# Kernel tuning notes

Measured on AMD Instinct MI355X. Metric: run time of the kernel, lower is better.

The kernel has to match this reference:

```python
import jax, jax.numpy as jnp
import numpy as np

B, D, HGT, WID = 32, 512, 8, 32   # batch, channels, feature map H, W
T = HGT * WID                     # 256 spatial tokens
NH, L, MAXLEN = 8, 2, 25          # heads, encoder layers, max text len


def _ln(x, s, b, eps=1e-5):
    m = jnp.mean(x, -1, keepdims=True)
    v = jnp.mean((x - m) ** 2, -1, keepdims=True)
    return (x - m) * jax.lax.rsqrt(v + eps) * s + b


def setup_inputs() -> dict:
    key = jax.random.key(0)
    ks = jax.random.split(key, 16)
    w = lambda k, shp: jax.random.normal(k, shp, jnp.float32) * 0.02
    return {
        "x": jax.random.normal(ks[0], (B, D, HGT, WID), jnp.float32),
        "encoder_word_pos": jnp.arange(T, dtype=jnp.int32),
        "gsrm_word_pos": jnp.arange(MAXLEN, dtype=jnp.int32),
        # encoder positional table
        "pos_table": w(ks[1], (T, D)),
        # per-layer encoder params (stacked over L)
        "ln1_s": jnp.ones((L, D), jnp.float32), "ln1_b": jnp.zeros((L, D), jnp.float32),
        "Wq": w(ks[2], (L, D, D)), "bq": jnp.zeros((L, D), jnp.float32),
        "Wk": w(ks[3], (L, D, D)), "bk": jnp.zeros((L, D), jnp.float32),
        "Wv": w(ks[4], (L, D, D)), "bv": jnp.zeros((L, D), jnp.float32),
        "Wo": w(ks[5], (L, D, D)), "bo": jnp.zeros((L, D), jnp.float32),
        "ln2_s": jnp.ones((L, D), jnp.float32), "ln2_b": jnp.zeros((L, D), jnp.float32),
        "W1": w(ks[6], (L, D, D)), "b1": jnp.zeros((L, D), jnp.float32),  # d_inner_hid = hidden_dim
        "W2": w(ks[7], (L, D, D)), "b2": jnp.zeros((L, D), jnp.float32),
        "lnf_s": jnp.ones((D,), jnp.float32), "lnf_b": jnp.zeros((D,), jnp.float32),
        # PVAM head params
        "fc0_w": w(ks[8], (D, D)), "fc0_b": jnp.zeros((D,), jnp.float32),
        "emb_table": w(ks[9], (MAXLEN, D)),
        "fc1_w": w(ks[10], (D,)),
    }


def _pvam(x, encoder_word_pos, gsrm_word_pos, pos_table,
          ln1_s, ln1_b, Wq, bq, Wk, bk, Wv, bv, Wo, bo,
          ln2_s, ln2_b, W1, b1, W2, b2, lnf_s, lnf_b,
          fc0_w, fc0_b, emb_table, fc1_w):
    b, c, h, wd = x.shape
    feat = x.reshape(b, c, h * wd).transpose(0, 2, 1)          # [b, t, c]
    # prepare encoder: scale + learned positional embedding (eval mode: no dropout)
    enc = feat * jnp.sqrt(jnp.float32(c)) + pos_table[encoder_word_pos]
    dk = c // NH
    scale = 1.0 / jnp.sqrt(jnp.float32(dk))
    for l in range(L):  # pre-norm transformer encoder (preprocess='n', postprocess='da')
        qin = _ln(enc, ln1_s[l], ln1_b[l])
        q = (qin @ Wq[l] + bq[l]).reshape(b, -1, NH, dk)
        k = (qin @ Wk[l] + bk[l]).reshape(b, -1, NH, dk)
        v = (qin @ Wv[l] + bv[l]).reshape(b, -1, NH, dk)
        p = jax.nn.softmax(jnp.einsum('bqhd,bkhd->bhqk', q, k) * scale, -1)
        o = jnp.einsum('bhqk,bkhd->bqhd', p, v).reshape(b, -1, c)
        enc = enc + (o @ Wo[l] + bo[l])
        y = _ln(enc, ln2_s[l], ln2_b[l])
        enc = enc + (jax.nn.relu(y @ W1[l] + b1[l]) @ W2[l] + b2[l])
    enc = _ln(enc, lnf_s, lnf_b)
    word_features = enc @ fc0_w + fc0_b                        # [b, t, c]
    word_pos = emb_table[gsrm_word_pos]                        # [max_len, c]
    # additive attention: tanh(broadcast add) -> scalar score -> softmax over t
    y = jnp.tanh(word_features[:, None, :, :] + word_pos[None, :, None, :])  # [b,max_len,t,c]
    attn = jax.nn.softmax(jnp.einsum('bmtc,c->bmt', y, fc1_w), -1)
    return jnp.einsum('bmt,btc->bmc', attn, word_features)    # [b, max_len, c]


def reference(x, encoder_word_pos, gsrm_word_pos, pos_table,
              ln1_s, ln1_b, Wq, bq, Wk, bk, Wv, bv, Wo, bo,
              ln2_s, ln2_b, W1, b1, W2, b2, lnf_s, lnf_b,
              fc0_w, fc0_b, emb_table, fc1_w):
    return _pvam(x, encoder_word_pos, gsrm_word_pos, pos_table,
                 ln1_s, ln1_b, Wq, bq, Wk, bk, Wv, bv, Wo, bo,
                 ln2_s, ln2_b, W1, b1, W2, b2, lnf_s, lnf_b,
                 fc0_w, fc0_b, emb_table, fc1_w)
```

## Files before the change

### kernel.cpp

```cpp
#include <hip/hip_runtime.h>
#include <math.h>

#define B_ 32
#define D_ 512
#define T_ 256
#define NH_ 8
#define DK_ 64
#define ML_ 25

typedef unsigned short ushort_t;
using short8 = __attribute__((ext_vector_type(8))) short;
using f32x4  = __attribute__((ext_vector_type(4))) float;

__device__ __forceinline__ ushort_t f2bf(float f) {
    unsigned u = __float_as_uint(f);
    unsigned r = (u + 0x7fffu + ((u >> 16) & 1u)) >> 16;
    return (ushort_t)r;
}
__device__ __forceinline__ float bf2f(ushort_t h) {
    return __uint_as_float(((unsigned)h) << 16);
}
__device__ __forceinline__ void gl16(const void* g, void* l) {
    __builtin_amdgcn_global_load_lds((const __attribute__((address_space(1))) void*)g,
                                     (__attribute__((address_space(3))) void*)l, 16, 0, 0);
}
#define ZERO4(v) { (v)[0]=0.f; (v)[1]=0.f; (v)[2]=0.f; (v)[3]=0.f; }

__global__ __launch_bounds__(256) void prep_kernel(const float* __restrict__ x,
                                                   const int* __restrict__ epos,
                                                   const float* __restrict__ pos,
                                                   float* __restrict__ enc) {
    __shared__ float ld[64][65];
    int tt = blockIdx.x, ct = blockIdx.y, b = blockIdx.z;
    int t0 = tt * 64, c0 = ct * 64;
    int tid = threadIdx.x;
    int r = tid >> 4, c4 = (tid & 15) << 2;
#pragma unroll
    for (int p = 0; p < 4; p++) {
        int row = p * 16 + r;
        float4 v = *(const float4*)(x + ((size_t)(b * D_ + c0 + row) * T_ + t0) + c4);
        ld[row][c4 + 0] = v.x; ld[row][c4 + 1] = v.y; ld[row][c4 + 2] = v.z; ld[row][c4 + 3] = v.w;
    }
    __syncthreads();
#pragma unroll
    for (int p = 0; p < 4; p++) {
        int tr = p * 16 + r;
        int ep = epos[t0 + tr];
        float4 pv = *(const float4*)(pos + (size_t)ep * D_ + c0 + c4);
        float4 o;
        o.x = ld[c4 + 0][tr] * 22.627417f + pv.x;
        o.y = ld[c4 + 1][tr] * 22.627417f + pv.y;
        o.z = ld[c4 + 2][tr] * 22.627417f + pv.z;
        o.w = ld[c4 + 3][tr] * 22.627417f + pv.w;
        *(float4*)(enc + (size_t)(b * T_ + t0 + tr) * D_ + c0 + c4) = o;
    }
}

__global__ __launch_bounds__(256) void convert_w_kernel(const float* __restrict__ Wq,
                                                        const float* __restrict__ Wk,
                                                        const float* __restrict__ Wv,
                                                        const float* __restrict__ Wo,
                                                        const float* __restrict__ W1,
                                                        const float* __restrict__ W2,
                                                        const float* __restrict__ fc0,
                                                        ushort_t* __restrict__ wt) {
    __shared__ float ld[64][65];
    int m = blockIdx.x >> 6;
    int tile = blockIdx.x & 63;
    int tn = tile >> 3, tk = tile & 7;
    int n0 = tn * 64, k0 = tk * 64;
    const float* src;
    if (m < 12) {
        int l = m / 6, w = m % 6;
        const float* bases[6] = {Wq, Wk, Wv, Wo, W1, W2};
        src = bases[w] + (size_t)l * D_ * D_;
    } else {
        src = fc0;
    }
    int tid = threadIdx.x;
    int r = tid >> 4, c4 = (tid & 15) << 2;
#pragma unroll
    for (int p = 0; p < 4; p++) {
        int row = p * 16 + r;
        float4 v = *(const float4*)(src + (size_t)(k0 + row) * D_ + n0 + c4);
        ld[row][c4 + 0] = v.x; ld[row][c4 + 1] = v.y; ld[row][c4 + 2] = v.z; ld[row][c4 + 3] = v.w;
    }
    __syncthreads();
    ushort_t* dsth = wt + (size_t)m * D_ * D_;
    ushort_t* dstl = wt + (size_t)13 * D_ * D_;
#pragma unroll
    for (int p = 0; p < 4; p++) {
        int n = p * 16 + r;
        int kc = c4;
        ushort_t h[4], lo[4];
#pragma unroll
        for (int i = 0; i < 4; i++) {
            float f = ld[kc + i][n];
            h[i] = f2bf(f);
            lo[i] = f2bf(f - bf2f(h[i]));
        }
        *(ushort4*)(dsth + (size_t)(n0 + n) * D_ + k0 + kc) = make_ushort4(h[0], h[1], h[2], h[3]);
        if (m == 12)
            *(ushort4*)(dstl + (size_t)(n0 + n) * D_ + k0 + kc) = make_ushort4(lo[0], lo[1], lo[2], lo[3]);
    }
}

template<bool LO>
__global__ __launch_bounds__(256) void ln_kernel(const float* __restrict__ x,
                                                 const float* __restrict__ s,
                                                 const float* __restrict__ b,
                                                 ushort_t* __restrict__ yh,
                                                 ushort_t* __restrict__ yl) {
    int wid = threadIdx.x >> 6, lane = threadIdx.x & 63;
    size_t row = (size_t)blockIdx.x * 4 + wid;
    const float4* xr = (const float4*)(x + row * D_);
    float4 v0 = xr[lane * 2], v1 = xr[lane * 2 + 1];
    float sum = v0.x + v0.y + v0.z + v0.w + v1.x + v1.y + v1.z + v1.w;
    for (int o = 32; o; o >>= 1) sum += __shfl_xor(sum, o);
    float mean = sum * (1.f / 512.f);
    float d[8] = {v0.x - mean, v0.y - mean, v0.z - mean, v0.w - mean,
                  v1.x - mean, v1.y - mean, v1.z - mean, v1.w - mean};
    float vs = 0.f;
#pragma unroll
    for (int i = 0; i < 8; i++) vs += d[i] * d[i];
    for (int o = 32; o; o >>= 1) vs += __shfl_xor(vs, o);
    float rs = 1.f / sqrtf(vs * (1.f / 512.f) + 1e-5f);
    const float4* s4 = (const float4*)s;
    const float4* b4 = (const float4*)b;
    float4 sa = s4[lane * 2], sb = s4[lane * 2 + 1];
    float4 ba = b4[lane * 2], bb = b4[lane * 2 + 1];
    float o8[8];
    o8[0] = d[0] * rs * sa.x + ba.x; o8[1] = d[1] * rs * sa.y + ba.y;
    o8[2] = d[2] * rs * sa.z + ba.z; o8[3] = d[3] * rs * sa.w + ba.w;
    o8[4] = d[4] * rs * sb.x + bb.x; o8[5] = d[5] * rs * sb.y + bb.y;
    o8[6] = d[6] * rs * sb.z + bb.z; o8[7] = d[7] * rs * sb.w + bb.w;
    ushort_t h[8];
#pragma unroll
    for (int i = 0; i < 8; i++) h[i] = f2bf(o8[i]);
    uint4 u;
    u.x = (unsigned)h[0] | ((unsigned)h[1] << 16);
    u.y = (unsigned)h[2] | ((unsigned)h[3] << 16);
    u.z = (unsigned)h[4] | ((unsigned)h[5] << 16);
    u.w = (unsigned)h[6] | ((unsigned)h[7] << 16);
    *(uint4*)(yh + row * D_ + lane * 8) = u;
    if (LO) {
        ushort_t l8[8];
#pragma unroll
        for (int i = 0; i < 8; i++) l8[i] = f2bf(o8[i] - bf2f(h[i]));
        uint4 ul;
        ul.x = (unsigned)l8[0] | ((unsigned)l8[1] << 16);
        ul.y = (unsigned)l8[2] | ((unsigned)l8[3] << 16);
        ul.z = (unsigned)l8[4] | ((unsigned)l8[5] << 16);
        ul.w = (unsigned)l8[6] | ((unsigned)l8[7] << 16);
        *(uint4*)(yl + row * D_ + lane * 8) = ul;
    }
}

template<int EPI>
__global__ __launch_bounds__(256) void gemm_kernel(const ushort_t* __restrict__ A0,
                                                   const ushort_t* __restrict__ A1,
                                                   const ushort_t* __restrict__ A2,
                                                   const ushort_t* __restrict__ B0,
                                                   const ushort_t* __restrict__ B1,
                                                   const ushort_t* __restrict__ B2,
                                                   int nseg, int nbn,
                                                   const float* __restrict__ bias,
                                                   const float* __restrict__ bias2,
                                                   const float* __restrict__ bias3,
                                                   const float* __restrict__ res,
                                                   float* __restrict__ outF,
                                                   ushort_t* __restrict__ outB) {
    __shared__ ushort_t As[3][128 * 64];
    __shared__ ushort_t Bs[3][64 * 64];
    int tid = threadIdx.x;
    int g = blockIdx.x;
    int per = gridDim.x >> 3;
    int lin = (g & 7) * per + (g >> 3);
    int bm = lin / nbn, bn = lin % nbn;

    int lane = tid & 63;
    int wid = tid >> 6;
    int wm = wid >> 1, wn = wid & 1;
    int xr = (lane & 7) << 3;

    f32x4 acc[4][2];
#pragma unroll
    for (int i = 0; i < 4; i++)
#pragma unroll
        for (int j = 0; j < 2; j++) ZERO4(acc[i][j]);

    int nt = nseg * 8;

#define STAGE(kt, buf)                                                                  \
    {                                                                                   \
        int seg_ = (kt) >> 3;                                                           \
        int k0_ = ((kt) & 7) * 64;                                                      \
        const ushort_t* Asg = seg_ == 0 ? A0 : (seg_ == 1 ? A1 : A2);                   \
        const ushort_t* Bsg = seg_ == 0 ? B0 : (seg_ == 1 ? B1 : B2);                   \
        _Pragma("unroll")                                                               \
        for (int it = 0; it < 4; it++) {                                                \
            int uu = tid + it * 256;                                                    \
            int row_ = uu >> 3;                                                         \
            int kb_ = (((uu & 7) ^ (row_ & 7)) << 3);                                   \
            gl16(Asg + (size_t)(bm * 128 + row_) * 512 + k0_ + kb_, &As[buf][uu * 8]);  \
        }                                                                               \
        _Pragma("unroll")                                                               \
        for (int it = 0; it < 2; it++) {                                                \
            int uu = tid + it * 256;                                                    \
            int row_ = uu >> 3;                                                         \
            int kb_ = (((uu & 7) ^ (row_ & 7)) << 3);                                   \
            gl16(Bsg + (size_t)(bn * 64 + row_) * 512 + k0_ + kb_, &Bs[buf][uu * 8]);   \
        }                                                                               \
    }

#define COMPUTE(bufc)                                                                        \
    {                                                                                        \
        _Pragma("unroll")                                                                    \
        for (int kc = 0; kc < 2; kc++) {                                                     \
            short8 a[4], b[2];                                                               \
            int koff = (kc * 32 + ((lane >> 4) << 3)) ^ xr;                                  \
            _Pragma("unroll")                                                                \
            for (int i = 0; i < 4; i++)                                                      \
                a[i] = *(const short8*)&As[bufc][(wm * 64 + i * 16 + (lane & 15)) * 64 + koff]; \
            _Pragma("unroll")                                                                \
            for (int j = 0; j < 2; j++)                                                      \
                b[j] = *(const short8*)&Bs[bufc][(wn * 32 + j * 16 + (lane & 15)) * 64 + koff]; \
            _Pragma("unroll")                                                                \
            for (int i = 0; i < 4; i++)                                                      \
                _Pragma("unroll")                                                            \
                for (int j = 0; j < 2; j++)                                                  \
                    acc[i][j] = __builtin_amdgcn_mfma_f32_16x16x32_bf16(a[i], b[j], acc[i][j], 0, 0, 0); \
        }                                                                                    \
    }

    STAGE(0, 0);
    if (nt > 1) STAGE(1, 1);
    asm volatile("s_waitcnt vmcnt(6)" ::: "memory");
    __builtin_amdgcn_s_barrier();

    int cur = 0;
    for (int t = 0; t < nt; t++) {
        if (t + 2 < nt) STAGE(t + 2, (cur + 2 >= 3 ? cur - 1 : cur + 2));
        COMPUTE(cur);
        if (t + 2 < nt) {
            asm volatile("s_waitcnt vmcnt(6)" ::: "memory");
        } else if (t + 1 < nt) {
            asm volatile("s_waitcnt vmcnt(0)" ::: "memory");
        }
        __builtin_amdgcn_s_barrier();
        cur = (cur == 2) ? 0 : cur + 1;
    }
#undef STAGE
#undef COMPUTE

#pragma unroll
    for (int i = 0; i < 4; i++) {
#pragma unroll
        for (int j = 0; j < 2; j++) {
            int r0 = bm * 128 + wm * 64 + i * 16 + ((lane >> 4) << 2);
            int col = bn * 64 + wn * 32 + j * 16 + (lane & 15);
            int seg = col >> 9;
            int ccol = col & 511;
            const float* bp = bias;
            if (EPI == 5) bp = (seg == 0) ? bias : (seg == 1 ? bias2 : bias3);
            float bc = bp[EPI == 5 ? ccol : col];
#pragma unroll
            for (int jj = 0; jj < 4; jj++) {
                float v = acc[i][j][jj] + bc;
                int row = r0 + jj;
                size_t idx = (size_t)row * 512 + col;
                if (EPI == 2) {
                    outF[idx] = v + res[idx];
                } else if (EPI == 3) {
                    outB[idx] = f2bf(fmaxf(v, 0.f));
                } else if (EPI == 4) {
                    outF[idx] = v;
                } else if (EPI == 5) {
                    if (seg < 2) {
                        outB[(size_t)seg * 4194304 + (size_t)row * 512 + ccol] = f2bf(v);
                    } else {
                        int bb2 = row >> 8, t2 = row & 255;
                        outB[(size_t)2 * 4194304 +
                             ((size_t)(bb2 * 8 + (ccol >> 6)) * 64 + (ccol & 63)) * 256 + t2] = f2bf(v);
                    }
                }
            }
        }
    }
}

__global__ __launch_bounds__(256) void attn_fused_kernel(const ushort_t* __restrict__ q,
                                                         const ushort_t* __restrict__ k,
                                                         const ushort_t* __restrict__ vt,
                                                         ushort_t* __restrict__ ao) {
    __shared__ ushort_t KVs[256 * 64];
    __shared__ ushort_t Ps[64 * 256];
    int tid = threadIdx.x;
    int lane = tid & 63;
    int wid = tid >> 6;
    int m0 = blockIdx.x * 64;
    int bh = blockIdx.y;
    int b = bh >> 3, h = bh & 7;
    int xr = (lane & 7) << 3;

#pragma unroll
    for (int it = 0; it < 8; it++) {
        int uu = tid + it * 256;
        int row = uu >> 3;
        int gx = ((uu & 7) ^ (row & 7)) << 3;
        gl16(k + (size_t)(b * T_ + row) * D_ + h * DK_ + gx, &KVs[uu * 8]);
    }
    short8 qa0, qa1;
    {
        int qrow = m0 + wid * 16 + (lane & 15);
        const ushort_t* qp = q + (size_t)(b * T_ + qrow) * D_ + h * DK_ + ((lane >> 4) << 3);
        qa0 = *(const short8*)(qp);
        qa1 = *(const short8*)(qp + 32);
    }
    f32x4 acc[16];
#pragma unroll
    for (int j = 0; j < 16; j++) ZERO4(acc[j]);
    asm volatile("s_waitcnt vmcnt(0)" ::: "memory");
    __syncthreads();

#pragma unroll
    for (int j = 0; j < 16; j++) {
        int krow = j * 16 + (lane & 15);
        short8 b0 = *(const short8*)&KVs[krow * 64 + ((((lane >> 4) << 3)) ^ xr)];
        short8 b1 = *(const short8*)&KVs[krow * 64 + ((32 + ((lane >> 4) << 3)) ^ xr)];
        acc[j] = __builtin_amdgcn_mfma_f32_16x16x32_bf16(qa0, b0, acc[j], 0, 0, 0);
        acc[j] = __builtin_amdgcn_mfma_f32_16x16x32_bf16(qa1, b1, acc[j], 0, 0, 0);
    }
    __syncthreads();

#pragma unroll
    for (int it = 0; it < 8; it++) {
        int uu = tid + it * 256;
        int row = uu >> 5;
        int gx = ((uu & 31) ^ (row & 7)) << 3;
        gl16(vt + ((size_t)bh * DK_ + row) * T_ + gx, &KVs[uu * 8]);
    }

    const float C = 0.125f * 1.44269504f;
#pragma unroll
    for (int jj = 0; jj < 4; jj++) {
        float mx = -1e30f;
#pragma unroll
        for (int j = 0; j < 16; j++) mx = fmaxf(mx, acc[j][jj]);
#pragma unroll
        for (int msk = 1; msk < 16; msk <<= 1) mx = fmaxf(mx, __shfl_xor(mx, msk));
        float sm = 0.f;
#pragma unroll
        for (int j = 0; j < 16; j++) {
            float e = __builtin_amdgcn_exp2f((acc[j][jj] - mx) * C);
            acc[j][jj] = e;
            sm += e;
        }
#pragma unroll
        for (int msk = 1; msk < 16; msk <<= 1) sm += __shfl_xor(sm, msk);
        float inv = 1.f / sm;
#pragma unroll
        for (int j = 0; j < 16; j++) acc[j][jj] *= inv;
    }
#pragma unroll
    for (int j = 0; j < 16; j++) {
#pragma unroll
        for (int jj = 0; jj < 4; jj++) {
            int row = wid * 16 + ((lane >> 4) << 2) + jj;
            int col = j * 16 + (lane & 15);
            Ps[row * 256 + (col ^ ((row & 7) << 3))] = f2bf(acc[j][jj]);
        }
    }
    asm volatile("s_waitcnt vmcnt(0)" ::: "memory");
    __syncthreads();

    int wm = wid >> 1, wn = wid & 1;
    f32x4 acc2[2][2];
#pragma unroll
    for (int i = 0; i < 2; i++)
#pragma unroll
        for (int j = 0; j < 2; j++) ZERO4(acc2[i][j]);
#pragma unroll
    for (int kc = 0; kc < 8; kc++) {
        int off = (kc * 32 + ((lane >> 4) << 3)) ^ xr;
        short8 a0 = *(const short8*)&Ps[(wm * 32 + (lane & 15)) * 256 + off];
        short8 a1 = *(const short8*)&Ps[(wm * 32 + 16 + (lane & 15)) * 256 + off];
        short8 b0 = *(const short8*)&KVs[(wn * 32 + (lane & 15)) * 256 + off];
        short8 b1 = *(const short8*)&KVs[(wn * 32 + 16 + (lane & 15)) * 256 + off];
        acc2[0][0] = __builtin_amdgcn_mfma_f32_16x16x32_bf16(a0, b0, acc2[0][0], 0, 0, 0);
        acc2[0][1] = __builtin_amdgcn_mfma_f32_16x16x32_bf16(a0, b1, acc2[0][1], 0, 0, 0);
        acc2[1][0] = __builtin_amdgcn_mfma_f32_16x16x32_bf16(a1, b0, acc2[1][0], 0, 0, 0);
        acc2[1][1] = __builtin_amdgcn_mfma_f32_16x16x32_bf16(a1, b1, acc2[1][1], 0, 0, 0);
    }
#pragma unroll
    for (int i = 0; i < 2; i++)
#pragma unroll
        for (int j = 0; j < 2; j++)
#pragma unroll
            for (int jj = 0; jj < 4; jj++)
                ao[(size_t)(b * T_ + m0 + wm * 32 + i * 16 + ((lane >> 4) << 2) + jj) * D_ +
                   h * DK_ + wn * 32 + j * 16 + (lane & 15)] = f2bf(acc2[i][j][jj]);
}

__global__ __launch_bounds__(256) void scores_kernel(const float* __restrict__ wf,
                                                     const int* __restrict__ gpos,
                                                     const float* __restrict__ emb,
                                                     const float* __restrict__ w1,
                                                     float* __restrict__ scores) {
    __shared__ float wpL[5][512];
    __shared__ float w1m2[512];
    const float K2 = 2.885390082f;
    int tid = threadIdx.x;
    int b = blockIdx.y;
    int mg = blockIdx.z * 5;
    int t = blockIdx.x * 32 + (tid >> 3);
    int cg = tid & 7;
    for (int idx = tid; idx < 5 * 128; idx += 256) {
        int m = idx >> 7, w4 = idx & 127;
        float4 v = *(const float4*)(emb + (size_t)gpos[mg + m] * D_ + (w4 << 2));
        v.x *= K2; v.y *= K2; v.z *= K2; v.w *= K2;
        *(float4*)&wpL[m][w4 << 2] = v;
    }
    if (tid < 128) {
        float4 v = *(const float4*)(w1 + (tid << 2));
        v.x *= -2.f; v.y *= -2.f; v.z *= -2.f; v.w *= -2.f;
        *(float4*)&w1m2[tid << 2] = v;
    }
    float4 wfs[16];
    float W1S = 0.f;
    const float* wfr = wf + (size_t)(b * T_ + t) * D_ + (cg << 2);
#pragma unroll
    for (int j = 0; j < 16; j++) {
        float4 v = *(const float4*)(wfr + (j << 5));
        wfs[j].x = v.x * K2; wfs[j].y = v.y * K2; wfs[j].z = v.z * K2; wfs[j].w = v.w * K2;
        float4 wv = *(const float4*)(w1 + (cg << 2) + (j << 5));
        W1S += wv.x + wv.y + wv.z + wv.w;
    }
    __syncthreads();
    float s[5] = {W1S, W1S, W1S, W1S, W1S};
#pragma unroll
    for (int j = 0; j < 16; j++) {
        float4 w14 = *(const float4*)&w1m2[(cg << 2) + (j << 5)];
#pragma unroll
        for (int m = 0; m < 5; m++) {
            float4 wp4 = *(const float4*)&wpL[m][(cg << 2) + (j << 5)];
            s[m] += w14.x * __builtin_amdgcn_rcpf(__builtin_amdgcn_exp2f(wfs[j].x + wp4.x) + 1.f);
            s[m] += w14.y * __builtin_amdgcn_rcpf(__builtin_amdgcn_exp2f(wfs[j].y + wp4.y) + 1.f);
            s[m] += w14.z * __builtin_amdgcn_rcpf(__builtin_amdgcn_exp2f(wfs[j].z + wp4.z) + 1.f);
            s[m] += w14.w * __builtin_amdgcn_rcpf(__builtin_amdgcn_exp2f(wfs[j].w + wp4.w) + 1.f);
        }
    }
#pragma unroll
    for (int m = 0; m < 5; m++) {
        s[m] += __shfl_xor(s[m], 1);
        s[m] += __shfl_xor(s[m], 2);
        s[m] += __shfl_xor(s[m], 4);
    }
    if (cg == 0) {
#pragma unroll
        for (int m = 0; m < 5; m++)
            scores[((size_t)b * ML_ + mg + m) * T_ + t] = s[m];
    }
}

__global__ __launch_bounds__(256) void softmax_kernel(float* __restrict__ sc) {
    int wid = threadIdx.x >> 6, lane = threadIdx.x & 63;
    size_t row = (size_t)blockIdx.x * 4 + wid;
    float4* p = (float4*)(sc + row * T_);
    float4 v = p[lane];
    float mx = fmaxf(fmaxf(v.x, v.y), fmaxf(v.z, v.w));
    for (int o = 32; o; o >>= 1) mx = fmaxf(mx, __shfl_xor(mx, o));
    float4 e;
    e.x = __expf(v.x - mx); e.y = __expf(v.y - mx);
    e.z = __expf(v.z - mx); e.w = __expf(v.w - mx);
    float sm = e.x + e.y + e.z + e.w;
    for (int o = 32; o; o >>= 1) sm += __shfl_xor(sm, o);
    float inv = 1.f / sm;
    e.x *= inv; e.y *= inv; e.z *= inv; e.w *= inv;
    p[lane] = e;
}

__global__ __launch_bounds__(256) void wsum_kernel(const float* __restrict__ attn,
                                                   const float* __restrict__ wf,
                                                   float* __restrict__ out) {
    __shared__ float at[T_][8];
    int tid = threadIdx.x;
    int b = blockIdx.y, m0 = blockIdx.x * 5;
#pragma unroll
    for (int q = 0; q < 5; q++) {
        float a = attn[((size_t)b * ML_ + m0 + q) * T_ + tid];
        at[tid][q] = a;
    }
    __syncthreads();
    int c0 = tid << 1;
    const float* wfb = wf + (size_t)b * T_ * D_ + c0;
    float acc[5][2] = {};
    for (int t = 0; t < T_; t++) {
        float2 v = *(const float2*)(wfb + (size_t)t * D_);
        float4 a4 = *(const float4*)&at[t][0];
        float a5 = at[t][4];
        acc[0][0] += a4.x * v.x; acc[0][1] += a4.x * v.y;
        acc[1][0] += a4.y * v.x; acc[1][1] += a4.y * v.y;
        acc[2][0] += a4.z * v.x; acc[2][1] += a4.z * v.y;
        acc[3][0] += a4.w * v.x; acc[3][1] += a4.w * v.y;
        acc[4][0] += a5 * v.x;   acc[4][1] += a5 * v.y;
    }
#pragma unroll
    for (int q = 0; q < 5; q++) {
        float2 o;
        o.x = acc[q][0]; o.y = acc[q][1];
        *(float2*)(out + ((size_t)b * ML_ + m0 + q) * D_ + c0) = o;
    }
}

extern "C" void kernel_launch(void* const* d_in, const int* in_sizes, int n_in,
                              void* d_out, int out_size, void* d_ws, size_t ws_size,
                              hipStream_t stream) {
    (void)in_sizes; (void)n_in; (void)out_size; (void)ws_size;
    const float* x        = (const float*)d_in[0];
    const int*   epos     = (const int*)d_in[1];
    const int*   gpos     = (const int*)d_in[2];
    const float* pos_tab  = (const float*)d_in[3];
    const float* ln1_s    = (const float*)d_in[4];
    const float* ln1_b    = (const float*)d_in[5];
    const float* Wq       = (const float*)d_in[6];
    const float* bq       = (const float*)d_in[7];
    const float* Wk       = (const float*)d_in[8];
    const float* bk       = (const float*)d_in[9];
    const float* Wv       = (const float*)d_in[10];
    const float* bv       = (const float*)d_in[11];
    const float* Wo       = (const float*)d_in[12];
    const float* bo       = (const float*)d_in[13];
    const float* ln2_s    = (const float*)d_in[14];
    const float* ln2_b    = (const float*)d_in[15];
    const float* W1       = (const float*)d_in[16];
    const float* b1       = (const float*)d_in[17];
    const float* W2       = (const float*)d_in[18];
    const float* b2       = (const float*)d_in[19];
    const float* lnf_s    = (const float*)d_in[20];
    const float* lnf_b    = (const float*)d_in[21];
    const float* fc0_w    = (const float*)d_in[22];
    const float* fc0_b    = (const float*)d_in[23];
    const float* emb      = (const float*)d_in[24];
    const float* fc1_w    = (const float*)d_in[25];

    char* ws = (char*)d_ws;
    float*    enc = (float*)(ws);
    ushort_t* hi  = (ushort_t*)(ws + 16777216);
    ushort_t* qb  = (ushort_t*)(ws + 25165824);
    ushort_t* kb  = (ushort_t*)(ws + 33554432);
    ushort_t* lo  = (ushort_t*)(ws + 33554432);
    float*    scb = (float*)(ws + 33554432);
    ushort_t* vt  = (ushort_t*)(ws + 41943040);
    ushort_t* h1  = (ushort_t*)(ws + 41943040);
    ushort_t* ao  = (ushort_t*)(ws + 50331648);
    float*    wf  = (float*)(ws + 58720256);
    ushort_t* wt  = (ushort_t*)(ws + 75497472);
    const size_t WSL = (size_t)D_ * D_;

    convert_w_kernel<<<13 * 64, 256, 0, stream>>>(Wq, Wk, Wv, Wo, W1, W2, fc0_w, wt);
    prep_kernel<<<dim3(4, 8, 32), 256, 0, stream>>>(x, epos, pos_tab, enc);

    for (int l = 0; l < 2; l++) {
        size_t o1 = (size_t)l * D_;
        const ushort_t* WqkvT = wt + (l * 6 + 0) * WSL;
        const ushort_t* WoT = wt + (l * 6 + 3) * WSL;
        const ushort_t* W1T = wt + (l * 6 + 4) * WSL;
        const ushort_t* W2T = wt + (l * 6 + 5) * WSL;

        ln_kernel<false><<<2048, 256, 0, stream>>>(enc, ln1_s + o1, ln1_b + o1, hi, nullptr);
        gemm_kernel<5><<<1536, 256, 0, stream>>>(hi, nullptr, nullptr, WqkvT, nullptr, nullptr,
                                                 1, 24, bq + o1, bk + o1, bv + o1, nullptr, nullptr, qb);
        attn_fused_kernel<<<dim3(4, 256), 256, 0, stream>>>(qb, kb, vt, ao);
        gemm_kernel<2><<<512, 256, 0, stream>>>(ao, nullptr, nullptr, WoT, nullptr, nullptr,
                                                1, 8, bo + o1, nullptr, nullptr, enc, enc, nullptr);
        ln_kernel<false><<<2048, 256, 0, stream>>>(enc, ln2_s + o1, ln2_b + o1, hi, nullptr);
        gemm_kernel<3><<<512, 256, 0, stream>>>(hi, nullptr, nullptr, W1T, nullptr, nullptr,
                                                1, 8, b1 + o1, nullptr, nullptr, nullptr, nullptr, h1);
        gemm_kernel<2><<<512, 256, 0, stream>>>(h1, nullptr, nullptr, W2T, nullptr, nullptr,
                                                1, 8, b2 + o1, nullptr, nullptr, enc, enc, nullptr);
    }

    ln_kernel<true><<<2048, 256, 0, stream>>>(enc, lnf_s, lnf_b, hi, lo);
    gemm_kernel<4><<<512, 256, 0, stream>>>(hi, lo, hi, wt + 12 * WSL, wt + 12 * WSL, wt + 13 * WSL,
                                            3, 8, fc0_b, nullptr, nullptr, nullptr, wf, nullptr);
    scores_kernel<<<dim3(8, 32, 5), 256, 0, stream>>>(wf, gpos, emb, fc1_w, scb);
    softmax_kernel<<<200, 256, 0, stream>>>(scb);
    wsum_kernel<<<dim3(5, 32), 256, 0, stream>>>(scb, wf, (float*)d_out);
}
```

Measured before the change: 294.6 us.

## Shrink GEMM M-tile to 64 rows and fuse softmax into weighted-sum kernel

The GEMM block tile drops from 128x64 to 64x64, halving LDS staging and accumulators and doubling grid sizes. The aim is more blocks per GPU and more occupancy on these mid-sized GEMMs (M=8192), at the cost of lower per-block data reuse. The separate softmax kernel is removed, and the softmax is computed in wsum_kernel with block-level max and sum reductions before the weighted sum, saving one launch and one round trip through global memory.

```diff
diff --git a/kernel.cpp b/kernel.cpp
--- a/kernel.cpp
+++ b/kernel.cpp
@@ -170,7 +170,7 @@
                                                    const float* __restrict__ res,
                                                    float* __restrict__ outF,
                                                    ushort_t* __restrict__ outB) {
-    __shared__ ushort_t As[3][128 * 64];
+    __shared__ ushort_t As[3][64 * 64];
     __shared__ ushort_t Bs[3][64 * 64];
     int tid = threadIdx.x;
     int g = blockIdx.x;
@@ -183,9 +183,9 @@
     int wm = wid >> 1, wn = wid & 1;
     int xr = (lane & 7) << 3;
 
-    f32x4 acc[4][2];
-#pragma unroll
-    for (int i = 0; i < 4; i++)
+    f32x4 acc[2][2];
+#pragma unroll
+    for (int i = 0; i < 2; i++)
 #pragma unroll
         for (int j = 0; j < 2; j++) ZERO4(acc[i][j]);
 
@@ -198,11 +198,11 @@
         const ushort_t* Asg = seg_ == 0 ? A0 : (seg_ == 1 ? A1 : A2);                   \
         const ushort_t* Bsg = seg_ == 0 ? B0 : (seg_ == 1 ? B1 : B2);                   \
         _Pragma("unroll")                                                               \
-        for (int it = 0; it < 4; it++) {                                                \
+        for (int it = 0; it < 2; it++) {                                                \
             int uu = tid + it * 256;                                                    \
             int row_ = uu >> 3;                                                         \
             int kb_ = (((uu & 7) ^ (row_ & 7)) << 3);                                   \
-            gl16(Asg + (size_t)(bm * 128 + row_) * 512 + k0_ + kb_, &As[buf][uu * 8]);  \
+            gl16(Asg + (size_t)(bm * 64 + row_) * 512 + k0_ + kb_, &As[buf][uu * 8]);   \
         }                                                                               \
         _Pragma("unroll")                                                               \
         for (int it = 0; it < 2; it++) {                                                \
@@ -217,16 +217,16 @@
     {                                                                                        \
         _Pragma("unroll")                                                                    \
         for (int kc = 0; kc < 2; kc++) {                                                     \
-            short8 a[4], b[2];                                                               \
+            short8 a[2], b[2];                                                               \
             int koff = (kc * 32 + ((lane >> 4) << 3)) ^ xr;                                  \
             _Pragma("unroll")                                                                \
-            for (int i = 0; i < 4; i++)                                                      \
-                a[i] = *(const short8*)&As[bufc][(wm * 64 + i * 16 + (lane & 15)) * 64 + koff]; \
+            for (int i = 0; i < 2; i++)                                                      \
+                a[i] = *(const short8*)&As[bufc][(wm * 32 + i * 16 + (lane & 15)) * 64 + koff]; \
             _Pragma("unroll")                                                                \
             for (int j = 0; j < 2; j++)                                                      \
                 b[j] = *(const short8*)&Bs[bufc][(wn * 32 + j * 16 + (lane & 15)) * 64 + koff]; \
             _Pragma("unroll")                                                                \
-            for (int i = 0; i < 4; i++)                                                      \
+            for (int i = 0; i < 2; i++)                                                      \
                 _Pragma("unroll")                                                            \
                 for (int j = 0; j < 2; j++)                                                  \
                     acc[i][j] = __builtin_amdgcn_mfma_f32_16x16x32_bf16(a[i], b[j], acc[i][j], 0, 0, 0); \
@@ -234,8 +234,8 @@
     }
 
     STAGE(0, 0);
-    if (nt > 1) STAGE(1, 1);
-    asm volatile("s_waitcnt vmcnt(6)" ::: "memory");
+    STAGE(1, 1);
+    asm volatile("s_waitcnt vmcnt(4)" ::: "memory");
     __builtin_amdgcn_s_barrier();
 
     int cur = 0;
@@ -243,7 +243,7 @@
         if (t + 2 < nt) STAGE(t + 2, (cur + 2 >= 3 ? cur - 1 : cur + 2));
         COMPUTE(cur);
         if (t + 2 < nt) {
-            asm volatile("s_waitcnt vmcnt(6)" ::: "memory");
+            asm volatile("s_waitcnt vmcnt(4)" ::: "memory");
         } else if (t + 1 < nt) {
             asm volatile("s_waitcnt vmcnt(0)" ::: "memory");
         }
@@ -254,10 +254,10 @@
 #undef COMPUTE
 
 #pragma unroll
-    for (int i = 0; i < 4; i++) {
+    for (int i = 0; i < 2; i++) {
 #pragma unroll
         for (int j = 0; j < 2; j++) {
-            int r0 = bm * 128 + wm * 64 + i * 16 + ((lane >> 4) << 2);
+            int r0 = bm * 64 + wm * 32 + i * 16 + ((lane >> 4) << 2);
             int col = bn * 64 + wn * 32 + j * 16 + (lane & 15);
             int seg = col >> 9;
             int ccol = col & 511;
@@ -463,33 +463,40 @@
     }
 }
 
-__global__ __launch_bounds__(256) void softmax_kernel(float* __restrict__ sc) {
-    int wid = threadIdx.x >> 6, lane = threadIdx.x & 63;
-    size_t row = (size_t)blockIdx.x * 4 + wid;
-    float4* p = (float4*)(sc + row * T_);
-    float4 v = p[lane];
-    float mx = fmaxf(fmaxf(v.x, v.y), fmaxf(v.z, v.w));
-    for (int o = 32; o; o >>= 1) mx = fmaxf(mx, __shfl_xor(mx, o));
-    float4 e;
-    e.x = __expf(v.x - mx); e.y = __expf(v.y - mx);
-    e.z = __expf(v.z - mx); e.w = __expf(v.w - mx);
-    float sm = e.x + e.y + e.z + e.w;
-    for (int o = 32; o; o >>= 1) sm += __shfl_xor(sm, o);
-    float inv = 1.f / sm;
-    e.x *= inv; e.y *= inv; e.z *= inv; e.w *= inv;
-    p[lane] = e;
-}
-
-__global__ __launch_bounds__(256) void wsum_kernel(const float* __restrict__ attn,
+__global__ __launch_bounds__(256) void wsum_kernel(const float* __restrict__ scores,
                                                    const float* __restrict__ wf,
                                                    float* __restrict__ out) {
     __shared__ float at[T_][8];
+    __shared__ float redmax[4][8];
+    __shared__ float redsum[4][8];
     int tid = threadIdx.x;
+    int lane = tid & 63, wv = tid >> 6;
     int b = blockIdx.y, m0 = blockIdx.x * 5;
+    float s[5];
+#pragma unroll
+    for (int q = 0; q < 5; q++)
+        s[q] = scores[((size_t)b * ML_ + m0 + q) * T_ + tid];
 #pragma unroll
     for (int q = 0; q < 5; q++) {
-        float a = attn[((size_t)b * ML_ + m0 + q) * T_ + tid];
-        at[tid][q] = a;
+        float mx = s[q];
+        for (int o = 32; o; o >>= 1) mx = fmaxf(mx, __shfl_xor(mx, o));
+        if (lane == 0) redmax[wv][q] = mx;
+    }
+    __syncthreads();
+    float e[5];
+#pragma unroll
+    for (int q = 0; q < 5; q++) {
+        float m = fmaxf(fmaxf(redmax[0][q], redmax[1][q]), fmaxf(redmax[2][q], redmax[3][q]));
+        e[q] = __expf(s[q] - m);
+        float sm = e[q];
+        for (int o = 32; o; o >>= 1) sm += __shfl_xor(sm, o);
+        if (lane == 0) redsum[wv][q] = sm;
+    }
+    __syncthreads();
+#pragma unroll
+    for (int q = 0; q < 5; q++) {
+        float sm = redsum[0][q] + redsum[1][q] + redsum[2][q] + redsum[3][q];
+        at[tid][q] = e[q] / sm;
     }
     __syncthreads();
     int c0 = tid << 1;
@@ -569,22 +576,21 @@
         const ushort_t* W2T = wt + (l * 6 + 5) * WSL;
 
         ln_kernel<false><<<2048, 256, 0, stream>>>(enc, ln1_s + o1, ln1_b + o1, hi, nullptr);
-        gemm_kernel<5><<<1536, 256, 0, stream>>>(hi, nullptr, nullptr, WqkvT, nullptr, nullptr,
+        gemm_kernel<5><<<3072, 256, 0, stream>>>(hi, nullptr, nullptr, WqkvT, nullptr, nullptr,
                                                  1, 24, bq + o1, bk + o1, bv + o1, nullptr, nullptr, qb);
         attn_fused_kernel<<<dim3(4, 256), 256, 0, stream>>>(qb, kb, vt, ao);
-        gemm_kernel<2><<<512, 256, 0, stream>>>(ao, nullptr, nullptr, WoT, nullptr, nullptr,
-                                                1, 8, bo + o1, nullptr, nullptr, enc, enc, nullptr);
+        gemm_kernel<2><<<1024, 256, 0, stream>>>(ao, nullptr, nullptr, WoT, nullptr, nullptr,
+                                                 1, 8, bo + o1, nullptr, nullptr, enc, enc, nullptr);
         ln_kernel<false><<<2048, 256, 0, stream>>>(enc, ln2_s + o1, ln2_b + o1, hi, nullptr);
-        gemm_kernel<3><<<512, 256, 0, stream>>>(hi, nullptr, nullptr, W1T, nullptr, nullptr,
-                                                1, 8, b1 + o1, nullptr, nullptr, nullptr, nullptr, h1);
-        gemm_kernel<2><<<512, 256, 0, stream>>>(h1, nullptr, nullptr, W2T, nullptr, nullptr,
-                                                1, 8, b2 + o1, nullptr, nullptr, enc, enc, nullptr);
+        gemm_kernel<3><<<1024, 256, 0, stream>>>(hi, nullptr, nullptr, W1T, nullptr, nullptr,
+                                                 1, 8, b1 + o1, nullptr, nullptr, nullptr, nullptr, h1);
+        gemm_kernel<2><<<1024, 256, 0, stream>>>(h1, nullptr, nullptr, W2T, nullptr, nullptr,
+                                                 1, 8, b2 + o1, nullptr, nullptr, enc, enc, nullptr);
     }
 
     ln_kernel<true><<<2048, 256, 0, stream>>>(enc, lnf_s, lnf_b, hi, lo);
-    gemm_kernel<4><<<512, 256, 0, stream>>>(hi, lo, hi, wt + 12 * WSL, wt + 12 * WSL, wt + 13 * WSL,
-                                            3, 8, fc0_b, nullptr, nullptr, nullptr, wf, nullptr);
+    gemm_kernel<4><<<1024, 256, 0, stream>>>(hi, lo, hi, wt + 12 * WSL, wt + 12 * WSL, wt + 13 * WSL,
+                                             3, 8, fc0_b, nullptr, nullptr, nullptr, wf, nullptr);
     scores_kernel<<<dim3(8, 32, 5), 256, 0, stream>>>(wf, gpos, emb, fc1_w, scb);
-    softmax_kernel<<<200, 256, 0, stream>>>(scb);
     wsum_kernel<<<dim3(5, 32), 256, 0, stream>>>(scb, wf, (float*)d_out);
 }
```

Result: slower. 313.1 us (+6.3%).
